# Kernel optimization log

Measured on AMD Instinct MI355X. Metric: run time of the kernel, lower is better.

## Reference

```python
import jax, jax.numpy as jnp
import numpy as np

H = 512  # hidden_size
A = 1.0  # hard_sigm slope


def hard_sigm(a, x):
    return jnp.clip((a * x + 1.0) / 2.0, 0.0, 1.0)


def setup_inputs() -> dict:
    key = jax.random.key(0)
    ks = jax.random.split(key, 10)
    B = 8192
    bottom, top = 512, 512
    stdv = 1.0 / np.sqrt(H)
    u = lambda k, shp: jax.random.uniform(k, shp, jnp.float32, -stdv, stdv)
    return {
        "c": jax.random.normal(ks[0], (H, B), jnp.float32),
        "h_bottom": jax.random.normal(ks[1], (bottom, B), jnp.float32),
        "h": jax.random.normal(ks[2], (H, B), jnp.float32),
        "h_top": jax.random.normal(ks[3], (top, B), jnp.float32),
        "z": jax.random.uniform(ks[4], (1, B), jnp.float32),
        "z_bottom": jax.random.uniform(ks[5], (1, B), jnp.float32),
        "U_11": u(ks[6], (4 * H + 1, H)),
        "U_21": u(ks[7], (4 * H + 1, top)),
        "W_01": u(ks[8], (4 * H + 1, bottom)),
        "bias": u(ks[9], (4 * H + 1,)),
    }


def reference(c, h_bottom, h, h_top, z, z_bottom, U_11, U_21, W_01, bias):
    # z, z_bottom: (1, B) boundary indicators broadcast over the gate axis
    s_recur = (1.0 - z) * (U_11 @ h)          # (4H+1, B)
    s_topdown = z * (U_21 @ h_top)            # last_layer=False
    s_bottomup = z_bottom * (W_01 @ h_bottom)
    f_s = s_recur + s_topdown + s_bottomup + bias[:, None]

    f = jax.nn.sigmoid(f_s[0:H, :])
    i = jax.nn.sigmoid(f_s[H:2 * H, :])
    o = jax.nn.sigmoid(f_s[2 * H:3 * H, :])
    g = jnp.tanh(f_s[3 * H:4 * H, :])
    z_hat = hard_sigm(A, f_s[4 * H:4 * H + 1, :])  # (1, B)

    ig = i * g
    c_new = z * ig + (1.0 - z) * (1.0 - z_bottom) * c \
        + (1.0 - z) * z_bottom * (f * c + ig)
    tanh_c = jnp.tanh(c_new)
    h_new = z * o * tanh_c + (1.0 - z) * (1.0 - z_bottom) * h \
        + (1.0 - z) * z_bottom * o * tanh_c
    return (h_new, c_new, z_hat)
```

## Files before the change

kernel.cpp:

```cpp
#include <hip/hip_runtime.h>
#include <hip/hip_bf16.h>

#define HH 512
#define BB 8192
#define KK 1536
#define NT 48
#define HB 4194304
#define BLOB 8192

typedef __bf16 bhalf;
typedef __bf16 bf16x8 __attribute__((ext_vector_type(8)));
typedef float  f32x4  __attribute__((ext_vector_type(4)));

typedef __attribute__((address_space(1))) void* as1_t;
typedef __attribute__((address_space(3))) void* as3_t;

#define GLDS(src, dst) __builtin_amdgcn_global_load_lds((as1_t)(void*)(src), (as3_t)(void*)(dst), 16, 0, 0)
#define SBAR() asm volatile("s_barrier" ::: "memory")
#define VM8()  asm volatile("s_waitcnt vmcnt(8)" ::: "memory")
#define VM4()  asm volatile("s_waitcnt vmcnt(4)" ::: "memory")
#define VM0()  asm volatile("s_waitcnt vmcnt(0)" ::: "memory")


__global__ __launch_bounds__(256) void prep_x(
    const float* __restrict__ h, const float* __restrict__ ht,
    const float* __restrict__ hb, const float* __restrict__ z,
    const float* __restrict__ zb, bhalf* __restrict__ XtP)
{
    __shared__ float tile[32][257];
    const int tid = threadIdx.x;
    const int kt  = blockIdx.x;
    const int nt  = blockIdx.y;
    const int n   = nt * 256 + tid;
    const int kb  = kt * 32;

    const float* src; int kr; float scale;
    if (kb < 512)       { src = h;  kr = kb;        scale = 1.f - z[n]; }
    else if (kb < 1024) { src = ht; kr = kb - 512;  scale = z[n]; }
    else                { src = hb; kr = kb - 1024; scale = zb[n]; }

    #pragma unroll
    for (int kk = 0; kk < 32; ++kk)
        tile[kk][tid] = src[(size_t)(kr + kk) * BB + n] * scale;
    __syncthreads();

    bhalf* blob = XtP + (size_t)(nt * NT + kt) * BLOB;
    #pragma unroll
    for (int q = 0; q < 4; ++q) {
        const int s  = q * 256 + tid;
        const int rb = s >> 6, w = s & 63;
        const int hh = w >> 4, lrr = w & 15;
        const int nloc = rb * 16 + lrr, kloc = hh * 8;
        bf16x8 r;
        #pragma unroll
        for (int e = 0; e < 8; ++e) r[e] = (bhalf)tile[kloc + e][nloc];
        *(bf16x8*)(blob + s * 8) = r;
    }
}

__global__ __launch_bounds__(256) void prep_w(
    const float* __restrict__ U11, const float* __restrict__ U21,
    const float* __restrict__ W01, bhalf* __restrict__ WcP)
{
    const int o    = blockIdx.x * 4 + (threadIdx.x >> 6);
    const int lane = threadIdx.x & 63;
    const int g = o >> 9, j = o & 511;
    const int mp = 4 * j + g;
    const int mt = mp >> 8, rb = (mp >> 4) & 15, lrr = mp & 15;

    #pragma unroll
    for (int p = 0; p < 3; ++p) {
        const float* src = (p == 0) ? U11 : (p == 1) ? U21 : W01;
        const float* rp  = src + (size_t)o * 512 + lane * 8;
        float4 v0 = *(const float4*)rp;
        float4 v1 = *(const float4*)(rp + 4);
        bf16x8 r;
        r[0]=(bhalf)v0.x; r[1]=(bhalf)v0.y; r[2]=(bhalf)v0.z; r[3]=(bhalf)v0.w;
        r[4]=(bhalf)v1.x; r[5]=(bhalf)v1.y; r[6]=(bhalf)v1.z; r[7]=(bhalf)v1.w;
        const int kt = p * 16 + (lane >> 2);
        const int hh = lane & 3;
        *(bf16x8*)(WcP + (size_t)(mt * NT + kt) * BLOB
                   + rb * 512 + hh * 128 + lrr * 8) = r;
    }
}

__device__ __forceinline__ float sigmf(float x)    { return 1.f / (1.f + __expf(-x)); }
__device__ __forceinline__ float tanhfast(float x) { return 2.f / (1.f + __expf(-2.f * x)) - 1.f; }

__global__ __launch_bounds__(512, 2) void gemm_fused(
    const bhalf* __restrict__ WcP, const bhalf* __restrict__ XtP,
    const float* __restrict__ bias, const float* __restrict__ c_in,
    const float* __restrict__ h_in, const float* __restrict__ z,
    const float* __restrict__ zb, float* __restrict__ out)
{
    __shared__ bhalf As[4][BLOB];
    __shared__ bhalf Bs[4][BLOB];

    const int tid  = threadIdx.x;
    const int lane = tid & 63;
    const int wid  = tid >> 6;
    const int wm   = wid >> 2, wn = wid & 3;
    const int lr   = lane & 15, hi = lane >> 4;
    const int soff = hi * 128 + lr * 8;

    const int xcd = blockIdx.x & 7;
    const int i   = blockIdx.x >> 3;
    const int mt  = ((xcd & 3) << 1) | (i & 1);
    const int nt  = ((xcd >> 2) << 4) | (i >> 1);
    const int m0 = mt * 256, n0 = nt * 256;

    const bhalf* gA = WcP + (size_t)mt * (NT * BLOB) + tid * 8;
    const bhalf* gB = XtP + (size_t)nt * (NT * BLOB) + tid * 8;

    const bhalf* pA0 = &As[0][wm * 4096 + soff];
    const bhalf* pA1 = &As[1][wm * 4096 + soff];
    const bhalf* pA2 = &As[2][wm * 4096 + soff];
    const bhalf* pA3 = &As[3][wm * 4096 + soff];
    const bhalf* pB0 = &Bs[0][wn * 2048 + soff];
    const bhalf* pB1 = &Bs[1][wn * 2048 + soff];
    const bhalf* pB2 = &Bs[2][wn * 2048 + soff];
    const bhalf* pB3 = &Bs[3][wn * 2048 + soff];

#define STAGE(t, bf) do {                                                     \
        const bhalf* sa_ = gA + (size_t)(t) * BLOB;                           \
        const bhalf* sb_ = gB + (size_t)(t) * BLOB;                           \
        GLDS(sa_, &As[bf][tid * 8]); GLDS(sa_ + 4096, &As[bf][tid * 8 + 4096]); \
        GLDS(sb_, &Bs[bf][tid * 8]); GLDS(sb_ + 4096, &Bs[bf][tid * 8 + 4096]); \
    } while (0)

#define MF(mi, ni, A_, B_) acc[mi][ni] = \
    __builtin_amdgcn_mfma_f32_16x16x32_bf16(A_, B_, acc[mi][ni], 0, 0, 0)

#define CT(q) do {                                                            \
    bf16x8 b0 = *(const bf16x8*)(pB##q);                                      \
    bf16x8 b1 = *(const bf16x8*)(pB##q + 512);                                \
    bf16x8 b2 = *(const bf16x8*)(pB##q + 1024);                               \
    bf16x8 b3 = *(const bf16x8*)(pB##q + 1536);                               \
    bf16x8 a0 = *(const bf16x8*)(pA##q);                                      \
    bf16x8 a1 = *(const bf16x8*)(pA##q + 512);                                \
    bf16x8 a2 = *(const bf16x8*)(pA##q + 1024);                               \
    bf16x8 a3 = *(const bf16x8*)(pA##q + 1536);                               \
    bf16x8 a4 = *(const bf16x8*)(pA##q + 2048);                               \
    bf16x8 a5 = *(const bf16x8*)(pA##q + 2560);                               \
    bf16x8 a6 = *(const bf16x8*)(pA##q + 3072);                               \
    bf16x8 a7 = *(const bf16x8*)(pA##q + 3584);                               \
    __builtin_amdgcn_s_setprio(1);                                            \
    MF(0,0,a0,b0); MF(0,1,a0,b1); MF(0,2,a0,b2); MF(0,3,a0,b3);               \
    MF(1,0,a1,b0); MF(1,1,a1,b1); MF(1,2,a1,b2); MF(1,3,a1,b3);               \
    MF(2,0,a2,b0); MF(2,1,a2,b1); MF(2,2,a2,b2); MF(2,3,a2,b3);               \
    MF(3,0,a3,b0); MF(3,1,a3,b1); MF(3,2,a3,b2); MF(3,3,a3,b3);               \
    MF(4,0,a4,b0); MF(4,1,a4,b1); MF(4,2,a4,b2); MF(4,3,a4,b3);               \
    MF(5,0,a5,b0); MF(5,1,a5,b1); MF(5,2,a5,b2); MF(5,3,a5,b3);               \
    MF(6,0,a6,b0); MF(6,1,a6,b1); MF(6,2,a6,b2); MF(6,3,a6,b3);               \
    MF(7,0,a7,b0); MF(7,1,a7,b1); MF(7,2,a7,b2); MF(7,3,a7,b3);               \
    __builtin_amdgcn_s_setprio(0);                                            \
} while (0)

    f32x4 acc[8][4] = {};

    STAGE(0, 0); STAGE(1, 1); STAGE(2, 2);

    for (int base = 0; base < 44; base += 4) {
        VM8(); SBAR(); STAGE(base + 3, 3); CT(0);
        VM8(); SBAR(); STAGE(base + 4, 0); CT(1);
        VM8(); SBAR(); STAGE(base + 5, 1); CT(2);
        VM8(); SBAR(); STAGE(base + 6, 2); CT(3);
    }
    VM8(); SBAR(); STAGE(47, 3); CT(0);
    VM8(); SBAR(); CT(1);
    VM4(); SBAR(); CT(2);
    VM0(); SBAR(); CT(3);

    const int colbase = n0 + wn * 64 + lr;
    float zc[4], zbc[4];
    #pragma unroll
    for (int ni = 0; ni < 4; ++ni) {
        zc[ni]  = z[colbase + ni * 16];
        zbc[ni] = zb[colbase + ni * 16];
    }
    #pragma unroll
    for (int mi = 0; mi < 8; ++mi) {
        const int j = (m0 >> 2) + wm * 32 + mi * 4 + hi;
        const float bf_ = bias[j];
        const float bi_ = bias[512 + j];
        const float bo_ = bias[1024 + j];
        const float bg_ = bias[1536 + j];
        #pragma unroll
        for (int ni = 0; ni < 4; ++ni) {
            const int col = colbase + ni * 16;
            const size_t idx = (size_t)j * BB + col;
            const float cv = c_in[idx];
            const float hv = h_in[idx];
            const float fv = sigmf(acc[mi][ni][0] + bf_);
            const float iv = sigmf(acc[mi][ni][1] + bi_);
            const float ov = sigmf(acc[mi][ni][2] + bo_);
            const float gv = tanhfast(acc[mi][ni][3] + bg_);
            const float ig = iv * gv;
            const float zq = zc[ni], zbq = zbc[ni];
            const float cn = zq * ig + (1.f - zq) * (1.f - zbq) * cv
                           + (1.f - zq) * zbq * (fv * cv + ig);
            const float tc = tanhfast(cn);
            const float hn = (zq + (1.f - zq) * zbq) * ov * tc
                           + (1.f - zq) * (1.f - zbq) * hv;
            out[idx]      = hn;
            out[HB + idx] = cn;
        }
    }
}

__global__ __launch_bounds__(256) void zhat_k(
    const bhalf* __restrict__ XtP, const float* __restrict__ U11,
    const float* __restrict__ U21, const float* __restrict__ W01,
    const float* __restrict__ bias, float* __restrict__ out)
{
    __shared__ float wlds[1536];
    __shared__ float red[8][32];
    const int tid = threadIdx.x;
    for (int idx = tid; idx < 1536; idx += 256) {
        float v;
        if (idx < 512)       v = U11[1048576 + idx];
        else if (idx < 1024) v = U21[1048576 + idx - 512];
        else                 v = W01[1048576 + idx - 1024];
        wlds[idx] = v;
    }
    __syncthreads();

    const int col = tid & 31, kg = tid >> 5;
    const int n = blockIdx.x * 32 + col;
    const int nt = n >> 8, rb = (n >> 4) & 15, lrr = n & 15;
    const bhalf* base = XtP + (size_t)nt * (NT * BLOB) + rb * 512;

    float acc = 0.f;
    for (int kt = kg * 6; kt < kg * 6 + 6; ++kt) {
        #pragma unroll
        for (int hh = 0; hh < 4; ++hh) {
            bf16x8 v = *(const bf16x8*)(base + (size_t)kt * BLOB + hh * 128 + lrr * 8);
            #pragma unroll
            for (int e = 0; e < 8; ++e)
                acc += (float)v[e] * wlds[kt * 32 + hh * 8 + e];
        }
    }
    red[kg][col] = acc;
    __syncthreads();
    if (tid < 32) {
        float s = 0.f;
        #pragma unroll
        for (int k2 = 0; k2 < 8; ++k2) s += red[k2][tid];
        const float v = (s + bias[2048] + 1.f) * 0.5f;
        out[(size_t)2 * HB + blockIdx.x * 32 + tid] = fminf(fmaxf(v, 0.f), 1.f);
    }
}

extern "C" void kernel_launch(void* const* d_in, const int* in_sizes, int n_in,
                              void* d_out, int out_size, void* d_ws, size_t ws_size,
                              hipStream_t stream) {
    const float* c    = (const float*)d_in[0];
    const float* hb   = (const float*)d_in[1];
    const float* h    = (const float*)d_in[2];
    const float* ht   = (const float*)d_in[3];
    const float* z    = (const float*)d_in[4];
    const float* zb   = (const float*)d_in[5];
    const float* U11  = (const float*)d_in[6];
    const float* U21  = (const float*)d_in[7];
    const float* W01  = (const float*)d_in[8];
    const float* bias = (const float*)d_in[9];
    float* out = (float*)d_out;

    char* ws = (char*)d_ws;
    bhalf* XtP = (bhalf*)ws;
    bhalf* WcP = (bhalf*)(ws + 25165824);

    prep_x    <<<dim3(48, 32), 256, 0, stream>>>(h, ht, hb, z, zb, XtP);
    prep_w    <<<512, 256, 0, stream>>>(U11, U21, W01, WcP);
    gemm_fused<<<256, 512, 0, stream>>>(WcP, XtP, bias, c, h, z, zb, out);
    zhat_k    <<<256, 256, 0, stream>>>(XtP, U11, U21, W01, bias, out);
}
```

Before: 81.66 us.

## Halve GEMM N-tile to 128 with 256-thread blocks, triple buffering, LDS-staged c prefetch

Shrinks the fused GEMM block tile from 256x256 to 256x128, using 4 waves instead of 8 and 512 blocks instead of 256. The LDS pipeline drops from four to three stages to cut shared memory per block. The c_in tile for the epilogue is now prefetched into LDS with async global-to-LDS loads, overlapped with the last compute step, so the epilogue no longer reads it from global memory. The goal is more blocks for better CU coverage and load balance, at the cost of more A-tile traffic per output and a shallower prefetch pipeline.

```diff
diff --git a/kernel.cpp b/kernel.cpp
--- a/kernel.cpp
+++ b/kernel.cpp
@@ -17,8 +17,7 @@
 
 #define GLDS(src, dst) __builtin_amdgcn_global_load_lds((as1_t)(void*)(src), (as3_t)(void*)(dst), 16, 0, 0)
 #define SBAR() asm volatile("s_barrier" ::: "memory")
-#define VM8()  asm volatile("s_waitcnt vmcnt(8)" ::: "memory")
-#define VM4()  asm volatile("s_waitcnt vmcnt(4)" ::: "memory")
+#define VM6()  asm volatile("s_waitcnt vmcnt(6)" ::: "memory")
 #define VM0()  asm volatile("s_waitcnt vmcnt(0)" ::: "memory")
 
 
@@ -87,45 +86,49 @@
 __device__ __forceinline__ float sigmf(float x)    { return 1.f / (1.f + __expf(-x)); }
 __device__ __forceinline__ float tanhfast(float x) { return 2.f / (1.f + __expf(-2.f * x)) - 1.f; }
 
-__global__ __launch_bounds__(512, 2) void gemm_fused(
+__global__ __launch_bounds__(256, 2) void gemm_fused(
     const bhalf* __restrict__ WcP, const bhalf* __restrict__ XtP,
     const float* __restrict__ bias, const float* __restrict__ c_in,
     const float* __restrict__ h_in, const float* __restrict__ z,
     const float* __restrict__ zb, float* __restrict__ out)
 {
-    __shared__ bhalf As[4][BLOB];
-    __shared__ bhalf Bs[4][BLOB];
+    __shared__ bhalf As[3][BLOB];
+    __shared__ bhalf Bs[3][BLOB / 2];
 
     const int tid  = threadIdx.x;
     const int lane = tid & 63;
     const int wid  = tid >> 6;
-    const int wm   = wid >> 2, wn = wid & 3;
+    const int wm   = wid >> 1, wn = wid & 1;
     const int lr   = lane & 15, hi = lane >> 4;
     const int soff = hi * 128 + lr * 8;
 
     const int xcd = blockIdx.x & 7;
     const int i   = blockIdx.x >> 3;
     const int mt  = ((xcd & 3) << 1) | (i & 1);
-    const int nt  = ((xcd >> 2) << 4) | (i >> 1);
-    const int m0 = mt * 256, n0 = nt * 256;
+    const int nt2 = ((xcd >> 2) << 5) | (i >> 1);
+    const int m0 = mt * 256, n0 = nt2 * 128;
+    const int jb = mt * 64;
 
     const bhalf* gA = WcP + (size_t)mt * (NT * BLOB) + tid * 8;
-    const bhalf* gB = XtP + (size_t)nt * (NT * BLOB) + tid * 8;
+    const bhalf* gB = XtP + (size_t)(nt2 >> 1) * (NT * BLOB)
+                          + (nt2 & 1) * (BLOB / 2) + tid * 8;
 
     const bhalf* pA0 = &As[0][wm * 4096 + soff];
     const bhalf* pA1 = &As[1][wm * 4096 + soff];
     const bhalf* pA2 = &As[2][wm * 4096 + soff];
-    const bhalf* pA3 = &As[3][wm * 4096 + soff];
     const bhalf* pB0 = &Bs[0][wn * 2048 + soff];
     const bhalf* pB1 = &Bs[1][wn * 2048 + soff];
     const bhalf* pB2 = &Bs[2][wn * 2048 + soff];
-    const bhalf* pB3 = &Bs[3][wn * 2048 + soff];
 
 #define STAGE(t, bf) do {                                                     \
         const bhalf* sa_ = gA + (size_t)(t) * BLOB;                           \
         const bhalf* sb_ = gB + (size_t)(t) * BLOB;                           \
-        GLDS(sa_, &As[bf][tid * 8]); GLDS(sa_ + 4096, &As[bf][tid * 8 + 4096]); \
-        GLDS(sb_, &Bs[bf][tid * 8]); GLDS(sb_ + 4096, &Bs[bf][tid * 8 + 4096]); \
+        GLDS(sa_,        &As[bf][tid * 8]);                                   \
+        GLDS(sa_ + 2048, &As[bf][tid * 8 + 2048]);                            \
+        GLDS(sa_ + 4096, &As[bf][tid * 8 + 4096]);                            \
+        GLDS(sa_ + 6144, &As[bf][tid * 8 + 6144]);                            \
+        GLDS(sb_,        &Bs[bf][tid * 8]);                                   \
+        GLDS(sb_ + 2048, &Bs[bf][tid * 8 + 2048]);                            \
     } while (0)
 
 #define MF(mi, ni, A_, B_) acc[mi][ni] = \
@@ -158,20 +161,32 @@
 
     f32x4 acc[8][4] = {};
 
-    STAGE(0, 0); STAGE(1, 1); STAGE(2, 2);
-
-    for (int base = 0; base < 44; base += 4) {
-        VM8(); SBAR(); STAGE(base + 3, 3); CT(0);
-        VM8(); SBAR(); STAGE(base + 4, 0); CT(1);
-        VM8(); SBAR(); STAGE(base + 5, 1); CT(2);
-        VM8(); SBAR(); STAGE(base + 6, 2); CT(3);
-    }
-    VM8(); SBAR(); STAGE(47, 3); CT(0);
-    VM8(); SBAR(); CT(1);
-    VM4(); SBAR(); CT(2);
-    VM0(); SBAR(); CT(3);
-
+    STAGE(0, 0); STAGE(1, 1);
+
+    for (int t = 0; t < 45; t += 3) {
+        VM6(); SBAR(); STAGE(t + 2, 2); CT(0);
+        VM6(); SBAR(); STAGE(t + 3, 0); CT(1);
+        VM6(); SBAR(); STAGE(t + 4, 1); CT(2);
+    }
+    VM6(); SBAR(); STAGE(47, 2); CT(0);
+    VM6(); SBAR(); CT(1);
+    VM0(); SBAR();
+    {
+        float* AsF = (float*)&As[0][0];
+        #pragma unroll
+        for (int g = 0; g < 8; ++g) {
+            const int flat = g * 256 + tid;
+            const int row = flat >> 5, chunk = flat & 31;
+            GLDS(c_in + (size_t)(jb + row) * BB + n0 + chunk * 4,
+                 AsF + flat * 4);
+        }
+    }
+    CT(2);
+    VM0(); SBAR();
+
+    const float* cLDS = (const float*)&As[0][0];
     const int colbase = n0 + wn * 64 + lr;
+    const int jloc0   = wm * 32 + hi;
     float zc[4], zbc[4];
     #pragma unroll
     for (int ni = 0; ni < 4; ++ni) {
@@ -180,7 +195,8 @@
     }
     #pragma unroll
     for (int mi = 0; mi < 8; ++mi) {
-        const int j = (m0 >> 2) + wm * 32 + mi * 4 + hi;
+        const int jloc = jloc0 + mi * 4;
+        const int j    = jb + jloc;
         const float bf_ = bias[j];
         const float bi_ = bias[512 + j];
         const float bo_ = bias[1024 + j];
@@ -189,7 +205,7 @@
         for (int ni = 0; ni < 4; ++ni) {
             const int col = colbase + ni * 16;
             const size_t idx = (size_t)j * BB + col;
-            const float cv = c_in[idx];
+            const float cv = cLDS[jloc * 128 + (col - n0)];
             const float hv = h_in[idx];
             const float fv = sigmf(acc[mi][ni][0] + bf_);
             const float iv = sigmf(acc[mi][ni][1] + bi_);
@@ -272,6 +288,6 @@
 
     prep_x    <<<dim3(48, 32), 256, 0, stream>>>(h, ht, hb, z, zb, XtP);
     prep_w    <<<512, 256, 0, stream>>>(U11, U21, W01, WcP);
-    gemm_fused<<<256, 512, 0, stream>>>(WcP, XtP, bias, c, h, z, zb, out);
+    gemm_fused<<<512, 256, 0, stream>>>(WcP, XtP, bias, c, h, z, zb, out);
     zhat_k    <<<256, 256, 0, stream>>>(XtP, U11, U21, W01, bias, out);
 }
```

Measured after the change: 84.64 us. 1.04x slower.

## Halve GEMM N-tile, shrink LDS to double buffering, raise occupancy target

Applied to the files above, without the earlier changes.

The fused GEMM block tile shrinks from 256x256 to 256x128, so the grid grows to 512 blocks and each warp computes a 4x4 MFMA sub-tile instead of 8x4. The LDS pipeline drops from four stages to two, with a full vmcnt(0) wait before each k-step, and launch bounds now request four blocks per CU. The aim is more resident waves and smaller LDS and register footprints to hide latency. The cost is less data reuse per block, more B-matrix re-reads, and little load/compute overlap inside a block. The occupancy target forces a very tight register budget that may cause spills.

```diff
diff --git a/kernel.cpp b/kernel.cpp
--- a/kernel.cpp
+++ b/kernel.cpp
@@ -17,8 +17,6 @@
 
 #define GLDS(src, dst) __builtin_amdgcn_global_load_lds((as1_t)(void*)(src), (as3_t)(void*)(dst), 16, 0, 0)
 #define SBAR() asm volatile("s_barrier" ::: "memory")
-#define VM8()  asm volatile("s_waitcnt vmcnt(8)" ::: "memory")
-#define VM4()  asm volatile("s_waitcnt vmcnt(4)" ::: "memory")
 #define VM0()  asm volatile("s_waitcnt vmcnt(0)" ::: "memory")
 
 
@@ -87,45 +85,44 @@
 __device__ __forceinline__ float sigmf(float x)    { return 1.f / (1.f + __expf(-x)); }
 __device__ __forceinline__ float tanhfast(float x) { return 2.f / (1.f + __expf(-2.f * x)) - 1.f; }
 
-__global__ __launch_bounds__(512, 2) void gemm_fused(
+__global__ __launch_bounds__(512, 4) void gemm_fused(
     const bhalf* __restrict__ WcP, const bhalf* __restrict__ XtP,
     const float* __restrict__ bias, const float* __restrict__ c_in,
     const float* __restrict__ h_in, const float* __restrict__ z,
     const float* __restrict__ zb, float* __restrict__ out)
 {
-    __shared__ bhalf As[4][BLOB];
-    __shared__ bhalf Bs[4][BLOB];
+    __shared__ bhalf As[2][BLOB];
+    __shared__ bhalf Bs[2][BLOB / 2];
 
     const int tid  = threadIdx.x;
     const int lane = tid & 63;
     const int wid  = tid >> 6;
-    const int wm   = wid >> 2, wn = wid & 3;
+    const int wm   = wid >> 1, wn = wid & 1;
     const int lr   = lane & 15, hi = lane >> 4;
     const int soff = hi * 128 + lr * 8;
 
     const int xcd = blockIdx.x & 7;
     const int i   = blockIdx.x >> 3;
     const int mt  = ((xcd & 3) << 1) | (i & 1);
-    const int nt  = ((xcd >> 2) << 4) | (i >> 1);
-    const int m0 = mt * 256, n0 = nt * 256;
+    const int nt2 = ((xcd >> 2) << 5) | (i >> 1);
+    const int n0 = nt2 * 128;
+    const int jb = mt * 64;
 
     const bhalf* gA = WcP + (size_t)mt * (NT * BLOB) + tid * 8;
-    const bhalf* gB = XtP + (size_t)nt * (NT * BLOB) + tid * 8;
-
-    const bhalf* pA0 = &As[0][wm * 4096 + soff];
-    const bhalf* pA1 = &As[1][wm * 4096 + soff];
-    const bhalf* pA2 = &As[2][wm * 4096 + soff];
-    const bhalf* pA3 = &As[3][wm * 4096 + soff];
+    const bhalf* gB = XtP + (size_t)(nt2 >> 1) * (NT * BLOB)
+                          + (nt2 & 1) * (BLOB / 2) + tid * 8;
+
+    const bhalf* pA0 = &As[0][wm * 2048 + soff];
+    const bhalf* pA1 = &As[1][wm * 2048 + soff];
     const bhalf* pB0 = &Bs[0][wn * 2048 + soff];
     const bhalf* pB1 = &Bs[1][wn * 2048 + soff];
-    const bhalf* pB2 = &Bs[2][wn * 2048 + soff];
-    const bhalf* pB3 = &Bs[3][wn * 2048 + soff];
 
 #define STAGE(t, bf) do {                                                     \
         const bhalf* sa_ = gA + (size_t)(t) * BLOB;                           \
         const bhalf* sb_ = gB + (size_t)(t) * BLOB;                           \
-        GLDS(sa_, &As[bf][tid * 8]); GLDS(sa_ + 4096, &As[bf][tid * 8 + 4096]); \
-        GLDS(sb_, &Bs[bf][tid * 8]); GLDS(sb_ + 4096, &Bs[bf][tid * 8 + 4096]); \
+        GLDS(sa_,        &As[bf][tid * 8]);                                   \
+        GLDS(sa_ + 4096, &As[bf][tid * 8 + 4096]);                            \
+        GLDS(sb_,        &Bs[bf][tid * 8]);                                   \
     } while (0)
 
 #define MF(mi, ni, A_, B_) acc[mi][ni] = \
@@ -140,38 +137,27 @@
     bf16x8 a1 = *(const bf16x8*)(pA##q + 512);                                \
     bf16x8 a2 = *(const bf16x8*)(pA##q + 1024);                               \
     bf16x8 a3 = *(const bf16x8*)(pA##q + 1536);                               \
-    bf16x8 a4 = *(const bf16x8*)(pA##q + 2048);                               \
-    bf16x8 a5 = *(const bf16x8*)(pA##q + 2560);                               \
-    bf16x8 a6 = *(const bf16x8*)(pA##q + 3072);                               \
-    bf16x8 a7 = *(const bf16x8*)(pA##q + 3584);                               \
     __builtin_amdgcn_s_setprio(1);                                            \
     MF(0,0,a0,b0); MF(0,1,a0,b1); MF(0,2,a0,b2); MF(0,3,a0,b3);               \
     MF(1,0,a1,b0); MF(1,1,a1,b1); MF(1,2,a1,b2); MF(1,3,a1,b3);               \
     MF(2,0,a2,b0); MF(2,1,a2,b1); MF(2,2,a2,b2); MF(2,3,a2,b3);               \
     MF(3,0,a3,b0); MF(3,1,a3,b1); MF(3,2,a3,b2); MF(3,3,a3,b3);               \
-    MF(4,0,a4,b0); MF(4,1,a4,b1); MF(4,2,a4,b2); MF(4,3,a4,b3);               \
-    MF(5,0,a5,b0); MF(5,1,a5,b1); MF(5,2,a5,b2); MF(5,3,a5,b3);               \
-    MF(6,0,a6,b0); MF(6,1,a6,b1); MF(6,2,a6,b2); MF(6,3,a6,b3);               \
-    MF(7,0,a7,b0); MF(7,1,a7,b1); MF(7,2,a7,b2); MF(7,3,a7,b3);               \
     __builtin_amdgcn_s_setprio(0);                                            \
 } while (0)
 
-    f32x4 acc[8][4] = {};
-
-    STAGE(0, 0); STAGE(1, 1); STAGE(2, 2);
-
-    for (int base = 0; base < 44; base += 4) {
-        VM8(); SBAR(); STAGE(base + 3, 3); CT(0);
-        VM8(); SBAR(); STAGE(base + 4, 0); CT(1);
-        VM8(); SBAR(); STAGE(base + 5, 1); CT(2);
-        VM8(); SBAR(); STAGE(base + 6, 2); CT(3);
-    }
-    VM8(); SBAR(); STAGE(47, 3); CT(0);
-    VM8(); SBAR(); CT(1);
-    VM4(); SBAR(); CT(2);
-    VM0(); SBAR(); CT(3);
+    f32x4 acc[4][4] = {};
+
+    STAGE(0, 0);
+
+    for (int t = 0; t < 46; t += 2) {
+        VM0(); SBAR(); STAGE(t + 1, 1); CT(0);
+        VM0(); SBAR(); STAGE(t + 2, 0); CT(1);
+    }
+    VM0(); SBAR(); STAGE(47, 1); CT(0);
+    VM0(); SBAR(); CT(1);
 
     const int colbase = n0 + wn * 64 + lr;
+    const int jloc0   = wm * 16 + hi;
     float zc[4], zbc[4];
     #pragma unroll
     for (int ni = 0; ni < 4; ++ni) {
@@ -179,8 +165,8 @@
         zbc[ni] = zb[colbase + ni * 16];
     }
     #pragma unroll
-    for (int mi = 0; mi < 8; ++mi) {
-        const int j = (m0 >> 2) + wm * 32 + mi * 4 + hi;
+    for (int mi = 0; mi < 4; ++mi) {
+        const int j = jb + jloc0 + mi * 4;
         const float bf_ = bias[j];
         const float bi_ = bias[512 + j];
         const float bo_ = bias[1024 + j];
@@ -272,6 +258,6 @@
 
     prep_x    <<<dim3(48, 32), 256, 0, stream>>>(h, ht, hb, z, zb, XtP);
     prep_w    <<<512, 256, 0, stream>>>(U11, U21, W01, WcP);
-    gemm_fused<<<256, 512, 0, stream>>>(WcP, XtP, bias, c, h, z, zb, out);
+    gemm_fused<<<512, 512, 0, stream>>>(WcP, XtP, bias, c, h, z, zb, out);
     zhat_k    <<<256, 256, 0, stream>>>(XtP, U11, U21, W01, bias, out);
 }
```

New measurement: 81.72 us. Within noise of the previous version (+0.1%).
